# Kernel tuning notes

Hardware: AMD Instinct MI355X
Metric: run time of the kernel (lower is better)

Reference implementation:

```python
import jax, jax.numpy as jnp
from jax import lax
import numpy as np

D_MODEL = 1024
D_STATE = 16    # N
D_CONV = 4     # K
EXPAND = 2
D_INNER = EXPAND * D_MODEL          # E = 2048
DT_RANK = -(-D_MODEL // 16)         # ceil(D/16) = 64
BATCH, SEQLEN = 2, 1024


def setup_inputs() -> dict:
    key = jax.random.key(0)
    ks = jax.random.split(key, 12)
    s_in = 1.0 / np.sqrt(D_MODEL)
    s_e = 1.0 / np.sqrt(D_INNER)
    s_r = 1.0 / np.sqrt(DT_RANK)
    x = jax.random.normal(ks[0], (BATCH, SEQLEN, D_MODEL), jnp.float32)
    ln_g = jnp.ones((D_MODEL,), jnp.float32)
    ln_b = jnp.zeros((D_MODEL,), jnp.float32)
    W_in = jax.random.normal(ks[1], (D_MODEL, 2 * D_INNER), jnp.float32) * s_in
    conv_w = jax.random.normal(ks[2], (D_INNER, D_CONV), jnp.float32) * (1.0 / np.sqrt(D_CONV))
    conv_b = jnp.zeros((D_INNER,), jnp.float32)
    W_xp = jax.random.normal(ks[3], (D_INNER, DT_RANK + 2 * D_STATE), jnp.float32) * s_e
    W_dt = jax.random.normal(ks[4], (DT_RANK, D_INNER), jnp.float32) * s_r
    # dt bias init so softplus(b_dt) ~ U[1e-3, 1e-1] (official mamba init)
    dt = jnp.exp(jax.random.uniform(ks[5], (D_INNER,)) * (np.log(0.1) - np.log(1e-3)) + np.log(1e-3))
    b_dt = dt + jnp.log(-jnp.expm1(-dt))  # inverse softplus
    A_log = jnp.log(jnp.broadcast_to(jnp.arange(1, D_STATE + 1, dtype=jnp.float32), (D_INNER, D_STATE)))
    D_param = jnp.ones((D_INNER,), jnp.float32)
    W_out = jax.random.normal(ks[6], (D_INNER, D_MODEL), jnp.float32) * s_e
    res_scale = jnp.ones((1,), jnp.float32)
    return dict(x=x, ln_g=ln_g, ln_b=ln_b, W_in=W_in, conv_w=conv_w, conv_b=conv_b,
                W_xp=W_xp, W_dt=W_dt, b_dt=b_dt, A_log=A_log, D_param=D_param,
                W_out=W_out, res_scale=res_scale)


def _mamba_block(x, ln_g, ln_b, W_in, conv_w, conv_b, W_xp, W_dt, b_dt,
                 A_log, D_param, W_out, res_scale):
    B, L, D = x.shape
    E, N, K, R = D_INNER, D_STATE, D_CONV, DT_RANK
    # --- prenorm (LayerNorm, eps=1e-5) ---
    mu = jnp.mean(x, axis=-1, keepdims=True)
    var = jnp.mean(jnp.square(x - mu), axis=-1, keepdims=True)
    xn = (x - mu) * lax.rsqrt(var + 1e-5) * ln_g + ln_b
    # --- in projection, split into ssm-input u and gate z ---
    xz = jnp.einsum('bld,de->ble', xn, W_in)
    u, z = jnp.split(xz, 2, axis=-1)                      # each [B,L,E]
    # --- causal depthwise conv1d over time + SiLU ---
    uc = u.transpose(0, 2, 1)                             # [B,E,L]
    conv = lax.conv_general_dilated(
        uc, conv_w[:, None, :],                           # [E,1,K]
        window_strides=(1,), padding=[(K - 1, 0)],
        feature_group_count=E,
        dimension_numbers=('NCH', 'OIH', 'NCH'))
    u2 = jax.nn.silu(conv + conv_b[None, :, None]).transpose(0, 2, 1)  # [B,L,E]
    # --- input-dependent dt, B, C ---
    x_dbl = jnp.einsum('ble,er->blr', u2, W_xp)           # [B,L,R+2N]
    dt_lo, Bm, Cm = x_dbl[..., :R], x_dbl[..., R:R + N], x_dbl[..., R + N:]
    dt = jax.nn.softplus(jnp.einsum('blr,re->ble', dt_lo, W_dt) + b_dt)  # [B,L,E]
    A = -jnp.exp(A_log)                                   # [E,N]
    # --- selective scan over time ---
    def step(h, inp):
        dt_t, B_t, C_t, u_t = inp                         # [B,E],[B,N],[B,N],[B,E]
        dA = jnp.exp(dt_t[..., None] * A)                 # [B,E,N]
        h = dA * h + (dt_t * u_t)[..., None] * B_t[:, None, :]
        y_t = jnp.einsum('ben,bn->be', h, C_t)
        return h, y_t
    h0 = jnp.zeros((B, E, N), x.dtype)
    xs = (dt.transpose(1, 0, 2), Bm.transpose(1, 0, 2),
          Cm.transpose(1, 0, 2), u2.transpose(1, 0, 2))
    _, ys = lax.scan(step, h0, xs)                        # ys: [L,B,E]
    y = ys.transpose(1, 0, 2) + u2 * D_param              # skip term D*u
    y = y * jax.nn.silu(z)                                # gating
    out = jnp.einsum('ble,ed->bld', y, W_out)
    # dropout is identity in eval mode
    return x + res_scale * out


def reference(x, ln_g, ln_b, W_in, conv_w, conv_b, W_xp, W_dt, b_dt,
              A_log, D_param, W_out, res_scale):
    return _mamba_block(x, ln_g, ln_b, W_in, conv_w, conv_b, W_xp, W_dt, b_dt,
                        A_log, D_param, W_out, res_scale)
```

## Files before the change

kernel.cpp:

```cpp
#include <hip/hip_runtime.h>
#include <hip/hip_bf16.h>

#define D_MODEL 1024
#define D_STATE 16
#define D_CONV  4
#define D_INNER 2048
#define DT_RANK 64
#define BATCH   2
#define SEQLEN  1024
#define NROWS   (BATCH * SEQLEN)
#define XDBL_W  (DT_RANK + 2 * D_STATE)
#define NCHUNK  64
#define LCHUNK  16
#define NCHAN   (BATCH * D_INNER)
#define KSPLIT_XDBL 8

typedef unsigned short ushort_t;
typedef __attribute__((ext_vector_type(8))) short bf16x8;
typedef __attribute__((ext_vector_type(4))) float f32x4;

__device__ __forceinline__ ushort_t f2bf(float f) {
    union { float f; unsigned u; } v; v.f = f;
    unsigned r = v.u + 0x7fffu + ((v.u >> 16) & 1u);
    return (ushort_t)(r >> 16);
}
__device__ __forceinline__ float bf2f(ushort_t h) {
    union { unsigned u; float f; } v; v.u = (unsigned)h << 16; return v.f;
}
__device__ __forceinline__ float fast_sigmoid(float z) {
    return __builtin_amdgcn_rcpf(1.f + __expf(-z));
}

#define PRO_LN1   2048
#define PRO_TIN1  6144
#define PRO_TOUT1 8192
#define PRO_TXP1  8448
#define PRO_TOTAL 8576

__device__ __forceinline__ void transpose_job(const float* __restrict__ W,
                                              ushort_t* __restrict__ Wt,
                                              int R, int Creal,
                                              int cx, int ry, int tid,
                                              float t[32][33])
{
    int c0 = cx * 32, r0 = ry * 32;
    int tx = tid & 31, ty = tid >> 5;
    int col = c0 + tx;
    #pragma unroll
    for (int i = 0; i < 32; i += 8) {
        float v = (col < Creal) ? W[(size_t)(r0 + ty + i) * Creal + col] : 0.f;
        t[ty + i][tx] = v;
    }
    __syncthreads();
    #pragma unroll
    for (int i = 0; i < 32; i += 8)
        Wt[(size_t)(c0 + ty + i) * R + r0 + tx] = f2bf(t[tx][ty + i]);
}

__global__ __launch_bounds__(256)
void prologue_kernel(const float* __restrict__ x, const float* __restrict__ g,
                     const float* __restrict__ bb, ushort_t* __restrict__ xnbf,
                     const float* __restrict__ W_in, ushort_t* __restrict__ WtIn,
                     const float* __restrict__ W_out, ushort_t* __restrict__ WtOut,
                     const float* __restrict__ W_xp, ushort_t* __restrict__ WtXp,
                     const float* __restrict__ W_dt, ushort_t* __restrict__ WtDt)
{
    __shared__ float t[32][33];
    __shared__ float red[8];
    int bid = blockIdx.x;
    int tid = threadIdx.x;

    if (bid < PRO_LN1) {
        const float* xr = x + (size_t)bid * D_MODEL;
        float4 v = reinterpret_cast<const float4*>(xr)[tid];
        float s  = v.x + v.y + v.z + v.w;
        float ss = v.x * v.x + v.y * v.y + v.z * v.z + v.w * v.w;
        #pragma unroll
        for (int off = 32; off; off >>= 1) {
            s  += __shfl_down(s, off);
            ss += __shfl_down(ss, off);
        }
        int wid = tid >> 6, lane = tid & 63;
        if (lane == 0) { red[wid] = s; red[4 + wid] = ss; }
        __syncthreads();
        if (tid == 0) {
            float st = 0.f, sst = 0.f;
            #pragma unroll
            for (int i = 0; i < 4; ++i) { st += red[i]; sst += red[4 + i]; }
            red[0] = st; red[4] = sst;
        }
        __syncthreads();
        float mu  = red[0] * (1.f / D_MODEL);
        float var = red[4] * (1.f / D_MODEL) - mu * mu;
        float inv = rsqrtf(var + 1e-5f);
        float4 gv = reinterpret_cast<const float4*>(g)[tid];
        float4 bv = reinterpret_cast<const float4*>(bb)[tid];
        ushort4 o;
        o.x = f2bf((v.x - mu) * inv * gv.x + bv.x);
        o.y = f2bf((v.y - mu) * inv * gv.y + bv.y);
        o.z = f2bf((v.z - mu) * inv * gv.z + bv.z);
        o.w = f2bf((v.w - mu) * inv * gv.w + bv.w);
        reinterpret_cast<ushort4*>(xnbf + (size_t)bid * D_MODEL)[tid] = o;
    } else if (bid < PRO_TIN1) {
        int j = bid - PRO_LN1;
        transpose_job(W_in, WtIn, D_MODEL, 2 * D_INNER, j & 127, j >> 7, tid, t);
    } else if (bid < PRO_TOUT1) {
        int j = bid - PRO_TIN1;
        transpose_job(W_out, WtOut, D_INNER, D_MODEL, j & 31, j >> 5, tid, t);
    } else if (bid < PRO_TXP1) {
        int j = bid - PRO_TOUT1;
        transpose_job(W_xp, WtXp, D_INNER, XDBL_W, j & 3, j >> 2, tid, t);
    } else {
        int j = bid - PRO_TXP1;
        transpose_job(W_dt, WtDt, DT_RANK, D_INNER, j & 63, j >> 6, tid, t);
    }
}

__device__ __forceinline__ void stage128x32(const ushort_t* __restrict__ gbase,
                                            size_t ld, ushort_t* ldsb, int tid)
{
    int l = tid & 63;
    int w = tid >> 6;
    int row = w * 16 + (l >> 2);
    int kg  = l & 3;
    char* lb = (char*)ldsb + w * 1024;
    const ushort_t* g0 = gbase + (size_t)row * ld + kg * 8;
    __builtin_amdgcn_global_load_lds(
        (const __attribute__((address_space(1))) unsigned*)g0,
        (__attribute__((address_space(3))) unsigned*)lb, 16, 0, 0);
    const ushort_t* g1 = g0 + (size_t)64 * ld;
    __builtin_amdgcn_global_load_lds(
        (const __attribute__((address_space(1))) unsigned*)g1,
        (__attribute__((address_space(3))) unsigned*)(lb + 4096), 16, 0, 0);
}

__device__ __forceinline__ void stage64x32(const ushort_t* __restrict__ gbase,
                                           size_t ld, ushort_t* ldsb, int tid)
{
    int l = tid & 63;
    int w = tid >> 6;
    int row = w * 16 + (l >> 2);
    int kg  = l & 3;
    char* lb = (char*)ldsb + w * 1024;
    const ushort_t* g0 = gbase + (size_t)row * ld + kg * 8;
    __builtin_amdgcn_global_load_lds(
        (const __attribute__((address_space(1))) unsigned*)g0,
        (__attribute__((address_space(3))) unsigned*)lb, 16, 0, 0);
}

__device__ __forceinline__ void stage64x64(const ushort_t* __restrict__ gbase,
                                           size_t ld, ushort_t* ldsb, int tid)
{
    int l = tid & 63;
    int w = tid >> 6;
    #pragma unroll
    for (int i = 0; i < 2; ++i) {
        int row = i * 32 + w * 8 + (l >> 3);
        const ushort_t* src = gbase + (size_t)row * ld + (l & 7) * 8;
        char* dst = (char*)ldsb + (i * 32 + w * 8) * 128;
        __builtin_amdgcn_global_load_lds(
            (const __attribute__((address_space(1))) unsigned*)src,
            (__attribute__((address_space(3))) unsigned*)dst, 16, 0, 0);
    }
}

__global__ __launch_bounds__(256)
void gemm_xz(const ushort_t* __restrict__ A, const ushort_t* __restrict__ Bt,
             ushort_t* __restrict__ C)
{
    __shared__ ushort_t As[128 * 32];
    __shared__ ushort_t Bs[128 * 32];
    const int K = D_MODEL, N = 2 * D_INNER;
    int bid = blockIdx.x;
    int swz = ((bid & 7) << 6) + (bid >> 3);
    int bx = swz & 31, by = swz >> 5;
    int tid = threadIdx.x;
    int l = tid & 63, wid = tid >> 6;
    int wr = wid >> 1, wc = wid & 1;
    int row0 = by * 128, col0 = bx * 128;

    f32x4 acc[4][4];
    #pragma unroll
    for (int m = 0; m < 4; ++m)
        #pragma unroll
        for (int n = 0; n < 4; ++n)
            acc[m][n] = (f32x4){0.f, 0.f, 0.f, 0.f};

    const ushort_t* Ab = A  + (size_t)row0 * K;
    const ushort_t* Bb = Bt + (size_t)col0 * K;
    int arow = wr * 64 + (l & 15);
    int brow = wc * 64 + (l & 15);
    int kb   = (l >> 4) * 8;

    for (int k0 = 0; k0 < K; k0 += 32) {
        stage128x32(Ab + k0, K, As, tid);
        stage128x32(Bb + k0, K, Bs, tid);
        __syncthreads();
        bf16x8 af[4], bfr[4];
        #pragma unroll
        for (int m = 0; m < 4; ++m)
            af[m] = *reinterpret_cast<const bf16x8*>(&As[(arow + m * 16) * 32 + kb]);
        #pragma unroll
        for (int n = 0; n < 4; ++n)
            bfr[n] = *reinterpret_cast<const bf16x8*>(&Bs[(brow + n * 16) * 32 + kb]);
        #pragma unroll
        for (int m = 0; m < 4; ++m)
            #pragma unroll
            for (int n = 0; n < 4; ++n)
                acc[m][n] = __builtin_amdgcn_mfma_f32_16x16x32_bf16(
                    af[m], bfr[n], acc[m][n], 0, 0, 0);
        __syncthreads();
    }

    int ro = (l >> 4) * 4, co = l & 15;
    #pragma unroll
    for (int m = 0; m < 4; ++m) {
        #pragma unroll
        for (int n = 0; n < 4; ++n) {
            int c = col0 + wc * 64 + n * 16 + co;
            #pragma unroll
            for (int reg = 0; reg < 4; ++reg) {
                int r = row0 + wr * 64 + m * 16 + ro + reg;
                C[(size_t)r * N + c] = f2bf(acc[m][n][reg]);
            }
        }
    }
}

__global__ __launch_bounds__(256)
void gemm_bf16_dt(const ushort_t* __restrict__ A, const ushort_t* __restrict__ Bt,
                  ushort_t* __restrict__ dtb, const float* __restrict__ bias)
{
    __shared__ ushort_t As[128 * 32];
    __shared__ ushort_t Bs[128 * 32];
    const int K = DT_RANK;
    int tid = threadIdx.x;
    int l = tid & 63, wid = tid >> 6;
    int wr = wid >> 1, wc = wid & 1;
    int row0 = blockIdx.y * 128, col0 = blockIdx.x * 128;

    f32x4 acc[4][4];
    #pragma unroll
    for (int m = 0; m < 4; ++m)
        #pragma unroll
        for (int n = 0; n < 4; ++n)
            acc[m][n] = (f32x4){0.f, 0.f, 0.f, 0.f};

    const ushort_t* Ab = A  + (size_t)row0 * K;
    const ushort_t* Bb = Bt + (size_t)col0 * K;
    int arow = wr * 64 + (l & 15);
    int brow = wc * 64 + (l & 15);
    int kb   = (l >> 4) * 8;

    #pragma unroll
    for (int k0 = 0; k0 < K; k0 += 32) {
        stage128x32(Ab + k0, K, As, tid);
        stage128x32(Bb + k0, K, Bs, tid);
        __syncthreads();
        bf16x8 af[4], bfr[4];
        #pragma unroll
        for (int m = 0; m < 4; ++m)
            af[m] = *reinterpret_cast<const bf16x8*>(&As[(arow + m * 16) * 32 + kb]);
        #pragma unroll
        for (int n = 0; n < 4; ++n)
            bfr[n] = *reinterpret_cast<const bf16x8*>(&Bs[(brow + n * 16) * 32 + kb]);
        #pragma unroll
        for (int m = 0; m < 4; ++m)
            #pragma unroll
            for (int n = 0; n < 4; ++n)
                acc[m][n] = __builtin_amdgcn_mfma_f32_16x16x32_bf16(
                    af[m], bfr[n], acc[m][n], 0, 0, 0);
        __syncthreads();
    }

    int ro = (l >> 4) * 4, co = l & 15;
    #pragma unroll
    for (int m = 0; m < 4; ++m) {
        #pragma unroll
        for (int n = 0; n < 4; ++n) {
            int c = col0 + wc * 64 + n * 16 + co;
            float bdt = bias[c];
            #pragma unroll
            for (int reg = 0; reg < 4; ++reg) {
                int r = row0 + wr * 64 + m * 16 + ro + reg;
                float v = acc[m][n][reg] + bdt;
                v = (v > 20.f) ? v : __logf(1.f + __expf(v));
                dtb[(size_t)r * D_INNER + c] = f2bf(v);
            }
        }
    }
}

__global__ __launch_bounds__(256)
void gemm_xdbl64(const ushort_t* __restrict__ A, const ushort_t* __restrict__ Bt,
                 float* __restrict__ parts)
{
    __shared__ ushort_t As[64 * 32];
    __shared__ ushort_t Bs[128 * 32];
    const int K = D_INNER;
    const int KS = D_INNER / KSPLIT_XDBL;
    int tid = threadIdx.x;
    int l = tid & 63, wid = tid >> 6;
    int wr = wid >> 1, wc = wid & 1;
    int row0 = blockIdx.y * 64;
    int kbeg = blockIdx.z * KS;

    f32x4 acc[2][4];
    #pragma unroll
    for (int m = 0; m < 2; ++m)
        #pragma unroll
        for (int n = 0; n < 4; ++n)
            acc[m][n] = (f32x4){0.f, 0.f, 0.f, 0.f};

    const ushort_t* Ab = A  + (size_t)row0 * K + kbeg;
    const ushort_t* Bb = Bt + kbeg;
    int arow = wr * 32 + (l & 15);
    int brow = wc * 64 + (l & 15);
    int kb   = (l >> 4) * 8;

    #pragma unroll
    for (int k0 = 0; k0 < KS; k0 += 32) {
        stage64x32(Ab + k0, K, As, tid);
        stage128x32(Bb + k0, K, Bs, tid);
        __syncthreads();
        bf16x8 af[2], bfr[4];
        #pragma unroll
        for (int m = 0; m < 2; ++m)
            af[m] = *reinterpret_cast<const bf16x8*>(&As[(arow + m * 16) * 32 + kb]);
        #pragma unroll
        for (int n = 0; n < 4; ++n)
            bfr[n] = *reinterpret_cast<const bf16x8*>(&Bs[(brow + n * 16) * 32 + kb]);
        #pragma unroll
        for (int m = 0; m < 2; ++m)
            #pragma unroll
            for (int n = 0; n < 4; ++n)
                acc[m][n] = __builtin_amdgcn_mfma_f32_16x16x32_bf16(
                    af[m], bfr[n], acc[m][n], 0, 0, 0);
        __syncthreads();
    }

    float* Cp = parts + (size_t)blockIdx.z * NROWS * XDBL_W;
    int ro = (l >> 4) * 4, co = l & 15;
    #pragma unroll
    for (int m = 0; m < 2; ++m) {
        #pragma unroll
        for (int n = 0; n < 4; ++n) {
            int c = wc * 64 + n * 16 + co;
            if (c >= XDBL_W) continue;
            #pragma unroll
            for (int reg = 0; reg < 4; ++reg) {
                int r = row0 + wr * 32 + m * 16 + ro + reg;
                Cp[(size_t)r * XDBL_W + c] = acc[m][n][reg];
            }
        }
    }
}

__global__ __launch_bounds__(256)
void gemm_out64(const ushort_t* __restrict__ A, const ushort_t* __restrict__ Bt,
                const float* __restrict__ x, const float* __restrict__ res_scale,
                float* __restrict__ out)
{
    __shared__ ushort_t As[64 * 64];
    __shared__ ushort_t Bs[64 * 64];
    const int K = D_INNER, N = D_MODEL;
    int bid = blockIdx.x;
    int swz = ((bid & 7) << 6) + (bid >> 3);
    int bx = swz & 15, by = swz >> 4;
    int tid = threadIdx.x;
    int l = tid & 63, wid = tid >> 6;
    int wr = wid >> 1, wc = wid & 1;
    int row0 = by * 64, col0 = bx * 64;

    f32x4 acc[2][2];
    #pragma unroll
    for (int m = 0; m < 2; ++m)
        #pragma unroll
        for (int n = 0; n < 2; ++n)
            acc[m][n] = (f32x4){0.f, 0.f, 0.f, 0.f};

    const ushort_t* Ab = A  + (size_t)row0 * K;
    const ushort_t* Bb = Bt + (size_t)col0 * K;
    int arow = wr * 32 + (l & 15);
    int brow = wc * 32 + (l & 15);
    int kb   = (l >> 4) * 8;

    for (int k0 = 0; k0 < K; k0 += 64) {
        stage64x64(Ab + k0, K, As, tid);
        stage64x64(Bb + k0, K, Bs, tid);
        __syncthreads();
        #pragma unroll
        for (int ks = 0; ks < 2; ++ks) {
            bf16x8 af[2], bfr[2];
            #pragma unroll
            for (int m = 0; m < 2; ++m)
                af[m] = *reinterpret_cast<const bf16x8*>(
                    &As[(arow + m * 16) * 64 + ks * 32 + kb]);
            #pragma unroll
            for (int n = 0; n < 2; ++n)
                bfr[n] = *reinterpret_cast<const bf16x8*>(
                    &Bs[(brow + n * 16) * 64 + ks * 32 + kb]);
            #pragma unroll
            for (int m = 0; m < 2; ++m)
                #pragma unroll
                for (int n = 0; n < 2; ++n)
                    acc[m][n] = __builtin_amdgcn_mfma_f32_16x16x32_bf16(
                        af[m], bfr[n], acc[m][n], 0, 0, 0);
        }
        __syncthreads();
    }

    float rs = res_scale[0];
    int ro = (l >> 4) * 4, co = l & 15;
    #pragma unroll
    for (int m = 0; m < 2; ++m) {
        #pragma unroll
        for (int n = 0; n < 2; ++n) {
            int c = col0 + wc * 32 + n * 16 + co;
            #pragma unroll
            for (int reg = 0; reg < 4; ++reg) {
                int r = row0 + wr * 32 + m * 16 + ro + reg;
                out[(size_t)r * N + c] = x[(size_t)r * N + c] + rs * acc[m][n][reg];
            }
        }
    }
}

__global__ __launch_bounds__(256)
void reduce_partials_kernel(const float* __restrict__ p, float* __restrict__ out,
                            ushort_t* __restrict__ out64bf, int n)
{
    int i = blockIdx.x * 256 + threadIdx.x;
    if (i >= n) return;
    float s = 0.f;
    #pragma unroll
    for (int k = 0; k < KSPLIT_XDBL; ++k) s += p[(size_t)k * n + i];
    out[i] = s;
    int r = i / XDBL_W, c = i - r * XDBL_W;
    if (c < DT_RANK) out64bf[r * DT_RANK + c] = f2bf(s);
}

__global__ __launch_bounds__(256)
void conv_silu_kernel(const ushort_t* __restrict__ xzbf, const float* __restrict__ cw,
                      const float* __restrict__ cb, ushort_t* __restrict__ u2bf)
{
    int idx4 = blockIdx.x * 256 + threadIdx.x;
    int e0 = (idx4 & 511) * 4;
    int l  = (idx4 >> 9) & (SEQLEN - 1);
    int b  = idx4 >> 19;
    size_t row = (size_t)b * SEQLEN + l;
    const ushort_t* base = xzbf + row * (2 * D_INNER) + e0;
    ushort4 r0 = {0,0,0,0}, r1 = {0,0,0,0}, r2 = {0,0,0,0}, r3;
    if (l >= 3) r0 = *reinterpret_cast<const ushort4*>(base - 3 * (size_t)(2 * D_INNER));
    if (l >= 2) r1 = *reinterpret_cast<const ushort4*>(base - 2 * (size_t)(2 * D_INNER));
    if (l >= 1) r2 = *reinterpret_cast<const ushort4*>(base - 1 * (size_t)(2 * D_INNER));
    r3 = *reinterpret_cast<const ushort4*>(base);
    const float4* cwv = reinterpret_cast<const float4*>(cw + (size_t)e0 * 4);
    float4 cb4 = *reinterpret_cast<const float4*>(cb + e0);
    const ushort_t* p0 = (const ushort_t*)&r0;
    const ushort_t* p1 = (const ushort_t*)&r1;
    const ushort_t* p2 = (const ushort_t*)&r2;
    const ushort_t* p3 = (const ushort_t*)&r3;
    const float* cbp = (const float*)&cb4;
    ushort4 o;
    ushort_t* op = (ushort_t*)&o;
    #pragma unroll
    for (int j = 0; j < 4; ++j) {
        float4 w = cwv[j];
        float a = cbp[j] + bf2f(p0[j]) * w.x + bf2f(p1[j]) * w.y
                         + bf2f(p2[j]) * w.z + bf2f(p3[j]) * w.w;
        op[j] = f2bf(a * fast_sigmoid(a));
    }
    reinterpret_cast<ushort4*>(u2bf)[idx4] = o;
}

__global__ __launch_bounds__(256)
void scan_partial_kernel(const ushort_t* __restrict__ dtb, const float* __restrict__ xdbl,
                         const ushort_t* __restrict__ u2bf,
                         const float* __restrict__ A_log,
                         float* __restrict__ hend, float* __restrict__ sumdt_buf)
{
    int idx = blockIdx.x * 256 + threadIdx.x;
    int p = idx & (NCHAN - 1);
    int c = idx >> 12;
    int b = p >> 11, e = p & (D_INNER - 1);

    float An[D_STATE];
    {
        const float4* ar = reinterpret_cast<const float4*>(A_log + (size_t)e * D_STATE);
        #pragma unroll
        for (int q = 0; q < 4; ++q) {
            float4 a4 = ar[q];
            An[q * 4 + 0] = -__expf(a4.x);
            An[q * 4 + 1] = -__expf(a4.y);
            An[q * 4 + 2] = -__expf(a4.z);
            An[q * 4 + 3] = -__expf(a4.w);
        }
    }
    float h[D_STATE];
    #pragma unroll
    for (int n = 0; n < D_STATE; ++n) h[n] = 0.f;
    float sdt = 0.f;

    size_t rowbase = (size_t)b * SEQLEN + c * LCHUNK;
    #pragma unroll
    for (int j = 0; j < LCHUNK; ++j) {
        size_t row = rowbase + j;
        float dt = bf2f(dtb[row * D_INNER + e]);
        float u  = bf2f(u2bf[row * D_INNER + e]);
        float dtu = dt * u;
        sdt += dt;
        const float4* xr = reinterpret_cast<const float4*>(xdbl + row * XDBL_W + DT_RANK);
        float Bv[D_STATE];
        #pragma unroll
        for (int q = 0; q < 4; ++q) {
            float4 b4 = xr[q];
            Bv[q * 4 + 0] = b4.x; Bv[q * 4 + 1] = b4.y;
            Bv[q * 4 + 2] = b4.z; Bv[q * 4 + 3] = b4.w;
        }
        #pragma unroll
        for (int n = 0; n < D_STATE; ++n)
            h[n] = __expf(dt * An[n]) * h[n] + dtu * Bv[n];
    }

    float4* hp = reinterpret_cast<float4*>(hend + ((size_t)p * NCHUNK + c) * D_STATE);
    #pragma unroll
    for (int q = 0; q < 4; ++q)
        hp[q] = (float4){h[q * 4 + 0], h[q * 4 + 1], h[q * 4 + 2], h[q * 4 + 3]};
    sumdt_buf[p * NCHUNK + c] = sdt;
}

__global__ __launch_bounds__(1024)
void scan_combine_kernel(const float* __restrict__ A_log,
                         const float* __restrict__ sumdt_buf,
                         float* __restrict__ hend )
{
    __shared__ float Ps[NCHUNK][D_STATE];
    __shared__ float Hs[NCHUNK][D_STATE];
    int tid = threadIdx.x;
    int c = tid >> 4, n = tid & 15;
    int p = blockIdx.x;
    int e = p & (D_INNER - 1);
    float An = -__expf(A_log[e * D_STATE + n]);
    float P = __expf(An * sumdt_buf[p * NCHUNK + c]);
    float H = hend[(size_t)p * (NCHUNK * D_STATE) + c * D_STATE + n];
    Ps[c][n] = P; Hs[c][n] = H;
    __syncthreads();
    #pragma unroll
    for (int d = 1; d < NCHUNK; d <<= 1) {
        float Pl = 1.f, Hl = 0.f;
        if (c >= d) { Pl = Ps[c - d][n]; Hl = Hs[c - d][n]; }
        __syncthreads();
        H = P * Hl + H;
        P = P * Pl;
        Ps[c][n] = P; Hs[c][n] = H;
        __syncthreads();
    }
    float carry = (c == 0) ? 0.f : Hs[c - 1][n];
    hend[(size_t)p * (NCHUNK * D_STATE) + c * D_STATE + n] = carry;
}

__global__ __launch_bounds__(256)
void scan_final_kernel(const ushort_t* __restrict__ dtb, const float* __restrict__ xdbl,
                       const ushort_t* __restrict__ xzbf, const ushort_t* __restrict__ u2bf,
                       ushort_t* __restrict__ ybf,
                       const float* __restrict__ A_log,
                       const float* __restrict__ D_param,
                       const float* __restrict__ hcarry)
{
    int idx = blockIdx.x * 256 + threadIdx.x;
    int p = idx & (NCHAN - 1);
    int c = idx >> 12;
    int b = p >> 11, e = p & (D_INNER - 1);
    float De = D_param[e];

    float An[D_STATE];
    {
        const float4* ar = reinterpret_cast<const float4*>(A_log + (size_t)e * D_STATE);
        #pragma unroll
        for (int q = 0; q < 4; ++q) {
            float4 a4 = ar[q];
            An[q * 4 + 0] = -__expf(a4.x);
            An[q * 4 + 1] = -__expf(a4.y);
            An[q * 4 + 2] = -__expf(a4.z);
            An[q * 4 + 3] = -__expf(a4.w);
        }
    }
    float h[D_STATE];
    {
        const float4* hp = reinterpret_cast<const float4*>(
            hcarry + ((size_t)p * NCHUNK + c) * D_STATE);
        #pragma unroll
        for (int q = 0; q < 4; ++q) {
            float4 h4 = hp[q];
            h[q * 4 + 0] = h4.x; h[q * 4 + 1] = h4.y;
            h[q * 4 + 2] = h4.z; h[q * 4 + 3] = h4.w;
        }
    }

    size_t rowbase = (size_t)b * SEQLEN + c * LCHUNK;
    #pragma unroll
    for (int j = 0; j < LCHUNK; ++j) {
        size_t row = rowbase + j;
        float dt = bf2f(dtb[row * D_INNER + e]);
        float u  = bf2f(u2bf[row * D_INNER + e]);
        float dtu = dt * u;
        const float4* xr = reinterpret_cast<const float4*>(xdbl + row * XDBL_W + DT_RANK);
        float Bv[D_STATE], Cv[D_STATE];
        #pragma unroll
        for (int q = 0; q < 4; ++q) {
            float4 b4 = xr[q];
            Bv[q * 4 + 0] = b4.x; Bv[q * 4 + 1] = b4.y;
            Bv[q * 4 + 2] = b4.z; Bv[q * 4 + 3] = b4.w;
            float4 c4 = xr[q + 4];
            Cv[q * 4 + 0] = c4.x; Cv[q * 4 + 1] = c4.y;
            Cv[q * 4 + 2] = c4.z; Cv[q * 4 + 3] = c4.w;
        }
        float y = 0.f;
        #pragma unroll
        for (int n = 0; n < D_STATE; ++n) {
            h[n] = __expf(dt * An[n]) * h[n] + dtu * Bv[n];
            y += h[n] * Cv[n];
        }
        float z  = bf2f(xzbf[row * (2 * D_INNER) + D_INNER + e]);
        float sz = z * fast_sigmoid(z);
        ybf[row * D_INNER + e] = f2bf((y + u * De) * sz);
    }
}

extern "C" void kernel_launch(void* const* d_in, const int* in_sizes, int n_in,
                              void* d_out, int out_size, void* d_ws, size_t ws_size,
                              hipStream_t stream)
{
    const float* x       = (const float*)d_in[0];
    const float* ln_g    = (const float*)d_in[1];
    const float* ln_b    = (const float*)d_in[2];
    const float* W_in    = (const float*)d_in[3];
    const float* conv_w  = (const float*)d_in[4];
    const float* conv_b  = (const float*)d_in[5];
    const float* W_xp    = (const float*)d_in[6];
    const float* W_dt    = (const float*)d_in[7];
    const float* b_dt    = (const float*)d_in[8];
    const float* A_log   = (const float*)d_in[9];
    const float* D_param = (const float*)d_in[10];
    const float* W_out   = (const float*)d_in[11];
    const float* res_sc  = (const float*)d_in[12];
    float* out = (float*)d_out;

    char* ws = (char*)d_ws;
    const size_t MB = 1024 * 1024;
    ushort_t* xzbf   = (ushort_t*)(ws);
    ushort_t* u2bf   = (ushort_t*)(ws + 16 * MB);
    ushort_t* dtb16  = (ushort_t*)(ws + 24 * MB);
    float*    xdbl   = (float*)(ws + 32 * MB);
    ushort_t* xdbl64 = (ushort_t*)(ws + 33 * MB);
    float*    hend   = (float*)(ws + 34 * MB);
    float*    sumdt  = (float*)(ws + 50 * MB);
    ushort_t* xnbf   = (ushort_t*)(ws + 51 * MB);
    ushort_t* WtIn   = (ushort_t*)(ws + 55 * MB);
    ushort_t* WtOut  = (ushort_t*)(ws + 63 * MB);
    ushort_t* WtXp   = (ushort_t*)(ws + 67 * MB);
    ushort_t* WtDt   = (ushort_t*)(ws + 67 * MB + 512 * 1024);
    ushort_t* ybf    = (ushort_t*)(ws + 68 * MB);
    float*    partsX = (float*)(ws + 76 * MB);

    prologue_kernel<<<PRO_TOTAL, 256, 0, stream>>>(
        x, ln_g, ln_b, xnbf, W_in, WtIn, W_out, WtOut, W_xp, WtXp, W_dt, WtDt);

    gemm_xz<<<512, 256, 0, stream>>>(xnbf, WtIn, xzbf);

    conv_silu_kernel<<<(BATCH * SEQLEN * D_INNER) / 1024, 256, 0, stream>>>(
        xzbf, conv_w, conv_b, u2bf);

    {
        dim3 grid(1, NROWS / 64, KSPLIT_XDBL);
        gemm_xdbl64<<<grid, 256, 0, stream>>>(u2bf, WtXp, partsX);
        reduce_partials_kernel<<<(NROWS * XDBL_W + 255) / 256, 256, 0, stream>>>(
            partsX, xdbl, xdbl64, NROWS * XDBL_W);
    }

    {
        dim3 grid(D_INNER / 128, NROWS / 128);
        gemm_bf16_dt<<<grid, 256, 0, stream>>>(xdbl64, WtDt, dtb16, b_dt);
    }

    scan_partial_kernel<<<(NCHAN * NCHUNK) / 256, 256, 0, stream>>>(
        dtb16, xdbl, u2bf, A_log, hend, sumdt);
    scan_combine_kernel<<<NCHAN, 1024, 0, stream>>>(A_log, sumdt, hend);
    scan_final_kernel<<<(NCHAN * NCHUNK) / 256, 256, 0, stream>>>(
        dtb16, xdbl, xzbf, u2bf, ybf, A_log, D_param, hend);

    gemm_out64<<<512, 256, 0, stream>>>(ybf, WtOut, x, res_sc, out);
}
```

Before: 163.6 us.

## Store scan chunk states in bf16 and double K tile in xz GEMM

```diff
diff --git a/kernel.cpp b/kernel.cpp
--- a/kernel.cpp
+++ b/kernel.cpp
@@ -17,6 +17,7 @@
 
 typedef unsigned short ushort_t;
 typedef __attribute__((ext_vector_type(8))) short bf16x8;
+typedef __attribute__((ext_vector_type(8))) unsigned short ushort8v;
 typedef __attribute__((ext_vector_type(4))) float f32x4;
 
 __device__ __forceinline__ ushort_t f2bf(float f) {
@@ -164,12 +165,28 @@
     }
 }
 
+__device__ __forceinline__ void stage128x64(const ushort_t* __restrict__ gbase,
+                                            size_t ld, ushort_t* ldsb, int tid)
+{
+    int l = tid & 63;
+    int w = tid >> 6;
+    #pragma unroll
+    for (int i = 0; i < 4; ++i) {
+        int row = i * 32 + w * 8 + (l >> 3);
+        const ushort_t* src = gbase + (size_t)row * ld + (l & 7) * 8;
+        char* dst = (char*)ldsb + (i * 32 + w * 8) * 128;
+        __builtin_amdgcn_global_load_lds(
+            (const __attribute__((address_space(1))) unsigned*)src,
+            (__attribute__((address_space(3))) unsigned*)dst, 16, 0, 0);
+    }
+}
+
 __global__ __launch_bounds__(256)
 void gemm_xz(const ushort_t* __restrict__ A, const ushort_t* __restrict__ Bt,
              ushort_t* __restrict__ C)
 {
-    __shared__ ushort_t As[128 * 32];
-    __shared__ ushort_t Bs[128 * 32];
+    __shared__ ushort_t As[128 * 64];
+    __shared__ ushort_t Bs[128 * 64];
     const int K = D_MODEL, N = 2 * D_INNER;
     int bid = blockIdx.x;
     int swz = ((bid & 7) << 6) + (bid >> 3);
@@ -192,23 +209,28 @@
     int brow = wc * 64 + (l & 15);
     int kb   = (l >> 4) * 8;
 
-    for (int k0 = 0; k0 < K; k0 += 32) {
-        stage128x32(Ab + k0, K, As, tid);
-        stage128x32(Bb + k0, K, Bs, tid);
-        __syncthreads();
-        bf16x8 af[4], bfr[4];
-        #pragma unroll
-        for (int m = 0; m < 4; ++m)
-            af[m] = *reinterpret_cast<const bf16x8*>(&As[(arow + m * 16) * 32 + kb]);
-        #pragma unroll
-        for (int n = 0; n < 4; ++n)
-            bfr[n] = *reinterpret_cast<const bf16x8*>(&Bs[(brow + n * 16) * 32 + kb]);
-        #pragma unroll
-        for (int m = 0; m < 4; ++m)
+    for (int k0 = 0; k0 < K; k0 += 64) {
+        stage128x64(Ab + k0, K, As, tid);
+        stage128x64(Bb + k0, K, Bs, tid);
+        __syncthreads();
+        #pragma unroll
+        for (int ks = 0; ks < 2; ++ks) {
+            bf16x8 af[4], bfr[4];
+            #pragma unroll
+            for (int m = 0; m < 4; ++m)
+                af[m] = *reinterpret_cast<const bf16x8*>(
+                    &As[(arow + m * 16) * 64 + ks * 32 + kb]);
             #pragma unroll
             for (int n = 0; n < 4; ++n)
-                acc[m][n] = __builtin_amdgcn_mfma_f32_16x16x32_bf16(
-                    af[m], bfr[n], acc[m][n], 0, 0, 0);
+                bfr[n] = *reinterpret_cast<const bf16x8*>(
+                    &Bs[(brow + n * 16) * 64 + ks * 32 + kb]);
+            #pragma unroll
+            for (int m = 0; m < 4; ++m)
+                #pragma unroll
+                for (int n = 0; n < 4; ++n)
+                    acc[m][n] = __builtin_amdgcn_mfma_f32_16x16x32_bf16(
+                        af[m], bfr[n], acc[m][n], 0, 0, 0);
+        }
         __syncthreads();
     }
 
@@ -478,7 +500,7 @@
 void scan_partial_kernel(const ushort_t* __restrict__ dtb, const float* __restrict__ xdbl,
                          const ushort_t* __restrict__ u2bf,
                          const float* __restrict__ A_log,
-                         float* __restrict__ hend, float* __restrict__ sumdt_buf)
+                         ushort_t* __restrict__ hend, float* __restrict__ sumdt_buf)
 {
     int idx = blockIdx.x * 256 + threadIdx.x;
     int p = idx & (NCHAN - 1);
@@ -523,17 +545,18 @@
             h[n] = __expf(dt * An[n]) * h[n] + dtu * Bv[n];
     }
 
-    float4* hp = reinterpret_cast<float4*>(hend + ((size_t)p * NCHUNK + c) * D_STATE);
-    #pragma unroll
-    for (int q = 0; q < 4; ++q)
-        hp[q] = (float4){h[q * 4 + 0], h[q * 4 + 1], h[q * 4 + 2], h[q * 4 + 3]};
+    ushort8v o0, o1;
+    #pragma unroll
+    for (int q = 0; q < 8; ++q) { o0[q] = f2bf(h[q]); o1[q] = f2bf(h[8 + q]); }
+    ushort8v* hp = reinterpret_cast<ushort8v*>(hend + ((size_t)p * NCHUNK + c) * D_STATE);
+    hp[0] = o0; hp[1] = o1;
     sumdt_buf[p * NCHUNK + c] = sdt;
 }
 
 __global__ __launch_bounds__(1024)
 void scan_combine_kernel(const float* __restrict__ A_log,
                          const float* __restrict__ sumdt_buf,
-                         float* __restrict__ hend )
+                         ushort_t* __restrict__ hend )
 {
     __shared__ float Ps[NCHUNK][D_STATE];
     __shared__ float Hs[NCHUNK][D_STATE];
@@ -543,7 +566,7 @@
     int e = p & (D_INNER - 1);
     float An = -__expf(A_log[e * D_STATE + n]);
     float P = __expf(An * sumdt_buf[p * NCHUNK + c]);
-    float H = hend[(size_t)p * (NCHUNK * D_STATE) + c * D_STATE + n];
+    float H = bf2f(hend[(size_t)p * (NCHUNK * D_STATE) + c * D_STATE + n]);
     Ps[c][n] = P; Hs[c][n] = H;
     __syncthreads();
     #pragma unroll
@@ -557,7 +580,7 @@
         __syncthreads();
     }
     float carry = (c == 0) ? 0.f : Hs[c - 1][n];
-    hend[(size_t)p * (NCHUNK * D_STATE) + c * D_STATE + n] = carry;
+    hend[(size_t)p * (NCHUNK * D_STATE) + c * D_STATE + n] = f2bf(carry);
 }
 
 __global__ __launch_bounds__(256)
@@ -566,7 +589,7 @@
                        ushort_t* __restrict__ ybf,
                        const float* __restrict__ A_log,
                        const float* __restrict__ D_param,
-                       const float* __restrict__ hcarry)
+                       const ushort_t* __restrict__ hcarry)
 {
     int idx = blockIdx.x * 256 + threadIdx.x;
     int p = idx & (NCHAN - 1);
@@ -588,14 +611,11 @@
     }
     float h[D_STATE];
     {
-        const float4* hp = reinterpret_cast<const float4*>(
+        const ushort8v* hp = reinterpret_cast<const ushort8v*>(
             hcarry + ((size_t)p * NCHUNK + c) * D_STATE);
-        #pragma unroll
-        for (int q = 0; q < 4; ++q) {
-            float4 h4 = hp[q];
-            h[q * 4 + 0] = h4.x; h[q * 4 + 1] = h4.y;
-            h[q * 4 + 2] = h4.z; h[q * 4 + 3] = h4.w;
-        }
+        ushort8v h0 = hp[0], h1 = hp[1];
+        #pragma unroll
+        for (int q = 0; q < 8; ++q) { h[q] = bf2f(h0[q]); h[8 + q] = bf2f(h1[q]); }
     }
 
     size_t rowbase = (size_t)b * SEQLEN + c * LCHUNK;
@@ -654,7 +674,7 @@
     ushort_t* dtb16  = (ushort_t*)(ws + 24 * MB);
     float*    xdbl   = (float*)(ws + 32 * MB);
     ushort_t* xdbl64 = (ushort_t*)(ws + 33 * MB);
-    float*    hend   = (float*)(ws + 34 * MB);
+    ushort_t* hend   = (ushort_t*)(ws + 34 * MB);
     float*    sumdt  = (float*)(ws + 50 * MB);
     ushort_t* xnbf   = (ushort_t*)(ws + 51 * MB);
     ushort_t* WtIn   = (ushort_t*)(ws + 55 * MB);
```

After: 162.9 us. No clear change (-0.5%).
